# Kernel optimization log

Hardware: AMD Instinct MI355X
Metric: run time of the kernel (lower is better)

Reference implementation:

```python
import jax, jax.numpy as jnp
import numpy as np

L = 5        # n_layers
H = 8        # heads
DH = 32      # dim_head = n_hidden // heads
D = 256      # n_hidden
KR = 4       # key_ratio
QKD = KR * DH  # 128, q/k feature dim
IN = 3       # fun_dim + space_dim
OUT = 1      # out_dim
N = 32768    # number of mesh points
EPS = 1e-5

def _ln(x, g, b):
    m = jnp.mean(x, axis=-1, keepdims=True)
    v = jnp.var(x, axis=-1, keepdims=True)
    return (x - m) * jax.lax.rsqrt(v + EPS) * g + b

def _gelu(x):
    return jax.nn.gelu(x, approximate=False)  # torch nn.GELU default (erf)

def setup_inputs() -> dict:
    key = jax.random.key(0)
    ks = iter(jax.random.split(key, 64))
    def w(*s):
        return jax.random.normal(next(ks), s, jnp.float32) * 0.02
    return {
        "x": jax.random.normal(next(ks), (N, IN), jnp.float32),
        # preprocess MLP: Linear(IN,2D)+GELU, Linear(2D,D)
        "pre_w1": w(IN, 2 * D), "pre_b1": jnp.zeros((2 * D,), jnp.float32),
        "pre_w2": w(2 * D, D), "pre_b2": jnp.zeros((D,), jnp.float32),
        "placeholder": jax.random.uniform(next(ks), (D,), jnp.float32) / D,
        # per-block params stacked over L
        "ln1_g": jnp.ones((L, D), jnp.float32), "ln1_b": jnp.zeros((L, D), jnp.float32),
        "inp_w": w(L, D, D), "inp_b": jnp.zeros((L, D), jnp.float32),
        "temp_q": jnp.full((L, H), 0.5, jnp.float32), "temp_k": jnp.full((L, H), 0.5, jnp.float32),
        "wq": w(L, DH, QKD), "wk": w(L, DH, QKD), "wv": w(L, DH, DH),
        "out_w1": w(L, D, D), "out_b1": jnp.zeros((L, D), jnp.float32),
        "out_w2": w(L, D, D), "out_b2": jnp.zeros((L, D), jnp.float32),
        "ln2_g": jnp.ones((L, D), jnp.float32), "ln2_b": jnp.zeros((L, D), jnp.float32),
        "mlp_w1": w(L, D, D), "mlp_b1": jnp.zeros((L, D), jnp.float32),  # mlp_ratio=1 -> hidden=D
        "mlp_w2": w(L, D, D), "mlp_b2": jnp.zeros((L, D), jnp.float32),
        # last-layer head
        "ln3_g": jnp.ones((D,), jnp.float32), "ln3_b": jnp.zeros((D,), jnp.float32),
        "head_w": w(D, OUT), "head_b": jnp.zeros((OUT,), jnp.float32),
    }

def reference(x, pre_w1, pre_b1, pre_w2, pre_b2, placeholder,
              ln1_g, ln1_b, inp_w, inp_b, temp_q, temp_k, wq, wk, wv,
              out_w1, out_b1, out_w2, out_b2, ln2_g, ln2_b,
              mlp_w1, mlp_b1, mlp_w2, mlp_b2, ln3_g, ln3_b, head_w, head_b):
    # preprocess + placeholder bias
    fx = _gelu(x[None] @ pre_w1 + pre_b1) @ pre_w2 + pre_b2  # [1, N, D]
    fx = fx + placeholder
    for i in range(L):
        # --- LinearNO attention block ---
        h = _ln(fx, ln1_g[i], ln1_b[i])
        xm = h @ inp_w[i] + inp_b[i]                       # [1, N, D]
        xm = xm.reshape(1, N, H, DH).transpose(0, 2, 1, 3)  # [1, H, N, DH]
        q = jnp.einsum('bhnd,de->bhne', xm, wq[i])          # [1, H, N, QKD]
        k = jnp.einsum('bhnd,de->bhne', xm, wk[i])          # [1, H, N, QKD]
        v = jnp.einsum('bhnd,dc->bhnc', xm, wv[i])          # [1, H, N, DH]
        tq = jnp.clip(temp_q[i], 0.1, 2.0)[None, :, None, None]
        tk = jnp.clip(temp_k[i], 0.1, 2.0)[None, :, None, None]
        q = jax.nn.softmax(q / tq, axis=-1)  # over feature dim
        k = jax.nn.softmax(k / tk, axis=-2)  # over point dim
        kv = jnp.einsum('bhnd,bhnc->bhdc', k, v)    # [1, H, QKD, DH]
        qkv = jnp.einsum('bhnd,bhdc->bhnc', q, kv)  # [1, H, N, DH]
        qkv = qkv.transpose(0, 2, 1, 3).reshape(1, N, D)
        attn = _gelu(qkv @ out_w1[i] + out_b1[i]) @ out_w2[i] + out_b2[i]
        fx = attn + fx
        # --- MLP block (n_layers=0, res=False: pre + post only) ---
        h2 = _ln(fx, ln2_g[i], ln2_b[i])
        fx = _gelu(h2 @ mlp_w1[i] + mlp_b1[i]) @ mlp_w2[i] + mlp_b2[i] + fx
    # last block head: mlp2(ln_3(fx))
    out = _ln(fx, ln3_g, ln3_b) @ head_w + head_b  # [1, N, OUT]
    return out[0]  # module returns fx[0]
```

## Files before the change

kernel.cpp:

```cpp
#include <hip/hip_runtime.h>
#include <hip/hip_bf16.h>
#include <math.h>

constexpr int NP  = 32768;
constexpr int HH  = 8;

typedef short bf16x8 __attribute__((ext_vector_type(8)));
typedef float f32x4  __attribute__((ext_vector_type(4)));

__device__ __forceinline__ float gelu_f(float x) {
    return 0.5f * x * (1.0f + erff(x * 0.70710678118654752f));
}

__device__ __forceinline__ unsigned short f2bf(float x) {
    union { float f; unsigned u; } v; v.f = x;
    unsigned r = v.u + 0x7fffu + ((v.u >> 16) & 1u);
    return (unsigned short)(r >> 16);
}

__device__ __forceinline__ float bf2f(unsigned short h) {
    union { unsigned u; float f; } v; v.u = ((unsigned)h) << 16;
    return v.f;
}

// ... 117 lines not shown
            float4 s0 = *(const float4*)sp;
            float4 s1 = *(const float4*)(sp + 4);
            float mean = (s0.x + s0.z + s1.x + s1.z) * (1.f / 256.f);
            float ex2  = (s0.y + s0.w + s1.y + s1.w) * (1.f / 256.f);
            rmean[tid] = mean;
            rrstd[tid] = rsqrtf(fmaxf(ex2 - mean * mean, 0.f) + 1e-5f);
        }
        __syncthreads();
    }

    f32x4 acc[4][4];
    #pragma unroll
    for (int i = 0; i < 4; ++i)
        #pragma unroll
        for (int j = 0; j < 4; ++j)
            acc[i][j] = (f32x4){0.f, 0.f, 0.f, 0.f};

    const int lane = tid & 63, wid = tid >> 6;
    const int wr = wid >> 1, wc = wid & 1;
    const int lrow = lane & 15, quad = lane >> 4;
    const int srow = tid >> 3;
    const int sch  = tid & 7;

    for (int kc = 0; kc < K; kc += 64) {
        if constexpr (GENA) {
            #pragma unroll
            for (int it = 0; it < 4; ++it) {
                int row = srow + it * 32;
                float x0 = x3s[row * 4 + 0], x1 = x3s[row * 4 + 1], x2 = x3s[row * 4 + 2];
                unsigned short pk[8];
                #pragma unroll
                for (int j = 0; j < 8; ++j) {
                    int k = kc + sch * 8 + j;
                    float t = x0 * w1s[k] + x1 * w1s[512 + k] + x2 * w1s[1024 + k] + b1s[k];
                    pk[j] = f2bf(gelu_f(t));
                }
                *(uint4*)&As[row * 64 + ((sch ^ (row & 7)) << 3)] = *(uint4*)pk;
            }
        } else if constexpr (AF32) {
            #pragma unroll
            for (int it = 0; it < 4; ++it) {
                int row = srow + it * 32;
                const float* ap = Af + (size_t)(rBase + row) * K + kc + sch * 8;
                float4 a0 = *(const float4*)ap;
                float4 a1 = *(const float4*)(ap + 4);
                unsigned short pk[8];
                pk[0] = f2bf(a0.x); pk[1] = f2bf(a0.y); pk[2] = f2bf(a0.z); pk[3] = f2bf(a0.w);
                pk[4] = f2bf(a1.x); pk[5] = f2bf(a1.y); pk[6] = f2bf(a1.z); pk[7] = f2bf(a1.w);
                *(uint4*)&As[row * 64 + ((sch ^ (row & 7)) << 3)] = *(uint4*)pk;
            }
        } else {
            #pragma unroll
            for (int it = 0; it < 4; ++it) {
                int row = srow + it * 32;
                uint4 av = *(const uint4*)(Ah + (size_t)(rBase + row) * K + kc + sch * 8);
                *(uint4*)&As[row * 64 + ((sch ^ (row & 7)) << 3)] = av;
            }
        }
        #pragma unroll
        for (int it = 0; it < 4; ++it) {
            int n = srow + it * 32;
            uint4 wv_ = *(const uint4*)(Wt + (size_t)(cBase + n) * K + kc + sch * 8);
            *(uint4*)&Bs[n * 64 + ((sch ^ (n & 7)) << 3)] = wv_;
        }
        __syncthreads();
        #pragma unroll
        for (int ks = 0; ks < 2; ++ks) {
            bf16x8 af[4], bfr[4];
            #pragma unroll
            for (int t = 0; t < 4; ++t) {
                int row = wr * 64 + t * 16 + lrow;
                af[t] = *(bf16x8*)&As[row * 64 + (((ks * 4 + quad) ^ (row & 7)) << 3)];
                int n = wc * 64 + t * 16 + lrow;
                bfr[t] = *(bf16x8*)&Bs[n * 64 + (((ks * 4 + quad) ^ (n & 7)) << 3)];
            }
            #pragma unroll
            for (int ti = 0; ti < 4; ++ti)
                #pragma unroll
                for (int tj = 0; tj < 4; ++tj)
                    acc[ti][tj] = __builtin_amdgcn_mfma_f32_16x16x32_bf16(
                        af[ti], bfr[tj], acc[ti][tj], 0, 0, 0);
        }
        __syncthreads();
    }

    float c1b[4], c2r[4];
    #pragma unroll
    for (int tj = 0; tj < 4; ++tj) {
        int gcol = cBase + wc * 64 + tj * 16 + lrow;
        float b = bias[gcol];
        if (bias2) b += bias2[gcol];
        if constexpr (LNFOLD) {
            c1b[tj] = c1v[gcol] + b;
            c2r[tj] = c2vec[gcol];
        } else {
            c1b[tj] = b;
            c2r[tj] = 0.f;
        }
    }
    #pragma unroll
    for (int ti = 0; ti < 4; ++ti) {
        #pragma unroll
        for (int r = 0; r < 4; ++r) {
            int rib = wr * 64 + ti * 16 + quad * 4 + r;
            int grow = rBase + rib;
            float mean = 0.f, rstd = 1.f;
            if constexpr (LNFOLD) { mean = rmean[rib]; rstd = rrstd[rib]; }
            float vv[4];
            #pragma unroll
            for (int tj = 0; tj < 4; ++tj) {
                float t = acc[ti][tj][r];
                float v;
                if constexpr (LNFOLD) v = rstd * (t - mean * c2r[tj]) + c1b[tj];
                else                  v = t + c1b[tj];
                if constexpr (DOGELU) v = gelu_f(v);
                vv[tj] = v;
            }
            if constexpr (RESID) {
                #pragma unroll
                for (int tj = 0; tj < 4; ++tj) {
                    int gcol = cBase + wc * 64 + tj * 16 + lrow;
                    vv[tj] += outF[(size_t)grow * 256 + gcol];
                }
            }
            if constexpr (STATS) {
                float rs = vv[0] + vv[1] + vv[2] + vv[3];
                float rq = vv[0]*vv[0] + vv[1]*vv[1] + vv[2]*vv[2] + vv[3]*vv[3];
                #pragma unroll
                for (int m = 1; m < 16; m <<= 1) {
                    rs += __shfl_xor(rs, m);
                    rq += __shfl_xor(rq, m);
                }
                if (lrow == 0) {
                    stats_out[(size_t)grow * 8 + (blockIdx.y * 2 + wc) * 2 + 0] = rs;
                    stats_out[(size_t)grow * 8 + (blockIdx.y * 2 + wc) * 2 + 1] = rq;
                }
            }
            #pragma unroll
            for (int tj = 0; tj < 4; ++tj) {
                int gcol = cBase + wc * 64 + tj * 16 + lrow;
                if constexpr (PERM) {
                    size_t pidx = (size_t)(gcol >> 5) * NP * 32 + (size_t)grow * 32 + (gcol & 31);
                    if (outF) outF[pidx] = vv[tj];
                    if (outH) outH[pidx] = f2bf(vv[tj]);
                } else {
                    if (outF) outF[(size_t)grow * 256 + gcol] = vv[tj];
                    if (outH) outH[(size_t)grow * 256 + gcol] = f2bf(vv[tj]);
                }
            }
        }
    }
}

template<bool AF32, bool LNFOLD>
__global__ __launch_bounds__(256) void gemm_lgl(
    const unsigned short* __restrict__ Ah, const float* __restrict__ Af,
    const unsigned short* __restrict__ W1t, const unsigned short* __restrict__ W2t,
    const float* __restrict__ b1, const float* __restrict__ b2,
    float* __restrict__ fx,
    const float* __restrict__ stats_in, float* __restrict__ stats_out,
    const float* __restrict__ c1v, const float* __restrict__ c2vec)
{
    __shared__ __align__(16) unsigned short As[64 * 64];
    __shared__ __align__(16) unsigned short Bs[256 * 64];
    __shared__ __align__(16) unsigned short Ts[64 * 256];
    __shared__ float rmean[LNFOLD ? 64 : 1];
    __shared__ float rrstd[LNFOLD ? 64 : 1];

    const int tid = threadIdx.x;
    const int rBase = blockIdx.x * 64;
    const int lane = tid & 63, wid = tid >> 6;
    const int lrow = lane & 15, quad = lane >> 4;

    if constexpr (LNFOLD) {
        if (tid < 64) {
            const float* sp = stats_in + (size_t)(rBase + tid) * 8;
            float4 s0 = *(const float4*)sp;
            float4 s1 = *(const float4*)(sp + 4);
            float mean = (s0.x + s0.z + s1.x + s1.z) * (1.f / 256.f);
            float ex2  = (s0.y + s0.w + s1.y + s1.w) * (1.f / 256.f);
            rmean[tid] = mean;
            rrstd[tid] = rsqrtf(fmaxf(ex2 - mean * mean, 0.f) + 1e-5f);
        }
    }

    f32x4 acc[4][4];
    #pragma unroll
    for (int i = 0; i < 4; ++i)
        #pragma unroll
        for (int j = 0; j < 4; ++j)
            acc[i][j] = (f32x4){0.f, 0.f, 0.f, 0.f};

    for (int kc = 0; kc < 256; kc += 64) {
        #pragma unroll
        for (int it = 0; it < 2; ++it) {
            int idx = tid + it * 256;
            int row = idx >> 3, sch = idx & 7;
            if constexpr (AF32) {
                const float* ap = Af + (size_t)(rBase + row) * 256 + kc + sch * 8;
                float4 a0 = *(const float4*)ap;
                float4 a1 = *(const float4*)(ap + 4);
                unsigned short pk[8];
                pk[0] = f2bf(a0.x); pk[1] = f2bf(a0.y); pk[2] = f2bf(a0.z); pk[3] = f2bf(a0.w);
                pk[4] = f2bf(a1.x); pk[5] = f2bf(a1.y); pk[6] = f2bf(a1.z); pk[7] = f2bf(a1.w);
                *(uint4*)&As[row * 64 + ((sch ^ (row & 7)) << 3)] = *(uint4*)pk;
            } else {
                uint4 av = *(const uint4*)(Ah + (size_t)(rBase + row) * 256 + kc + sch * 8);
                *(uint4*)&As[row * 64 + ((sch ^ (row & 7)) << 3)] = av;
            }
        }
        #pragma unroll
        for (int it = 0; it < 8; ++it) {
            int idx = tid + it * 256;
            int n = idx >> 3, sch = idx & 7;
            uint4 wv_ = *(const uint4*)(W1t + (size_t)n * 256 + kc + sch * 8);
            *(uint4*)&Bs[n * 64 + ((sch ^ (n & 7)) << 3)] = wv_;
        }
        __syncthreads();
        #pragma unroll
        for (int ks = 0; ks < 2; ++ks) {
            bf16x8 af[4], bfr[4];
            #pragma unroll
            for (int t = 0; t < 4; ++t) {
                int row = t * 16 + lrow;
                af[t] = *(bf16x8*)&As[row * 64 + (((ks * 4 + quad) ^ (row & 7)) << 3)];
                int n = wid * 64 + t * 16 + lrow;
                bfr[t] = *(bf16x8*)&Bs[n * 64 + (((ks * 4 + quad) ^ (n & 7)) << 3)];
            }
            #pragma unroll
            for (int ti = 0; ti < 4; ++ti)
                #pragma unroll
                for (int tj = 0; tj < 4; ++tj)
                    acc[ti][tj] = __builtin_amdgcn_mfma_f32_16x16x32_bf16(
                        af[ti], bfr[tj], acc[ti][tj], 0, 0, 0);
        }
        __syncthreads();
    }

    {
        float c1b[4], c2r[4];
        #pragma unroll
        for (int tj = 0; tj < 4; ++tj) {
            int gcol = wid * 64 + tj * 16 + lrow;
            if constexpr (LNFOLD) {
                c1b[tj] = c1v[gcol] + b1[gcol];
                c2r[tj] = c2vec[gcol];
            } else {
                c1b[tj] = b1[gcol];
                c2r[tj] = 0.f;
            }
        }
        #pragma unroll
        for (int ti = 0; ti < 4; ++ti) {
            #pragma unroll
            for (int r = 0; r < 4; ++r) {
                int row = ti * 16 + quad * 4 + r;
                float mean = 0.f, rstd = 1.f;
                if constexpr (LNFOLD) { mean = rmean[row]; rstd = rrstd[row]; }
                #pragma unroll
                for (int tj = 0; tj < 4; ++tj) {
                    float t = acc[ti][tj][r];
                    float v;
                    if constexpr (LNFOLD) v = rstd * (t - mean * c2r[tj]) + c1b[tj];
                    else                  v = t + c1b[tj];
                    v = gelu_f(v);
                    int col = wid * 64 + tj * 16 + lrow;
                    int ch = col >> 3;
                    Ts[row * 256 + ((ch ^ (row & 7)) << 3) + (col & 7)] = f2bf(v);
                }
            }
        }
    }
    __syncthreads();

    f32x4 acc2[4][4];
    #pragma unroll
    for (int i = 0; i < 4; ++i)
        #pragma unroll
        for (int j = 0; j < 4; ++j)
            acc2[i][j] = (f32x4){0.f, 0.f, 0.f, 0.f};

    for (int kc = 0; kc < 256; kc += 64) {
        #pragma unroll
        for (int it = 0; it < 8; ++it) {
            int idx = tid + it * 256;
            int n = idx >> 3, sch = idx & 7;
            uint4 wv_ = *(const uint4*)(W2t + (size_t)n * 256 + kc + sch * 8);
            *(uint4*)&Bs[n * 64 + ((sch ^ (n & 7)) << 3)] = wv_;
        }
        __syncthreads();
        #pragma unroll
        for (int ks = 0; ks < 2; ++ks) {
            bf16x8 af[4], bfr[4];
            #pragma unroll
            for (int t = 0; t < 4; ++t) {
                int row = t * 16 + lrow;
                int ch = (kc >> 3) + ks * 4 + quad;
                af[t] = *(bf16x8*)&Ts[row * 256 + ((ch ^ (row & 7)) << 3)];
                int n = wid * 64 + t * 16 + lrow;
                bfr[t] = *(bf16x8*)&Bs[n * 64 + (((ks * 4 + quad) ^ (n & 7)) << 3)];
            }
            #pragma unroll
            for (int ti = 0; ti < 4; ++ti)
                #pragma unroll
                for (int tj = 0; tj < 4; ++tj)
                    acc2[ti][tj] = __builtin_amdgcn_mfma_f32_16x16x32_bf16(
                        af[ti], bfr[tj], acc2[ti][tj], 0, 0, 0);
        }
        __syncthreads();
    }

    float bb[4];
    #pragma unroll
    for (int tj = 0; tj < 4; ++tj) bb[tj] = b2[wid * 64 + tj * 16 + lrow];
    #pragma unroll
    for (int ti = 0; ti < 4; ++ti) {
        #pragma unroll
        for (int r = 0; r < 4; ++r) {
            int grow = rBase + ti * 16 + quad * 4 + r;
            float vv[4];
            #pragma unroll
            for (int tj = 0; tj < 4; ++tj) {
                int gcol = wid * 64 + tj * 16 + lrow;
                vv[tj] = acc2[ti][tj][r] + bb[tj] + fx[(size_t)grow * 256 + gcol];
            }
            float rs = vv[0] + vv[1] + vv[2] + vv[3];
            float rq = vv[0]*vv[0] + vv[1]*vv[1] + vv[2]*vv[2] + vv[3]*vv[3];
            #pragma unroll
            for (int m = 1; m < 16; m <<= 1) {
                rs += __shfl_xor(rs, m);
                rq += __shfl_xor(rq, m);
            }
            if (lrow == 0) {
                stats_out[(size_t)grow * 8 + wid * 2 + 0] = rs;
                stats_out[(size_t)grow * 8 + wid * 2 + 1] = rq;
            }
            #pragma unroll
            for (int tj = 0; tj < 4; ++tj) {
                int gcol = wid * 64 + tj * 16 + lrow;
                fx[(size_t)grow * 256 + gcol] = vv[tj];
            }
        }
    }
}

__global__ __launch_bounds__(256) void kv6_kernel(
    const unsigned short* __restrict__ xm2h, const unsigned short* __restrict__ wkT,
    const unsigned short* __restrict__ wvT, const float* __restrict__ tk_arr,
    float* __restrict__ partials, int layer)
{
    __shared__ __align__(16) unsigned short xs[64 * 32];
    __shared__ __align__(16) unsigned short wks[128 * 32];
    __shared__ __align__(16) unsigned short wvs[32 * 32];
    __shared__ __align__(16) unsigned short els[128 * 72];
    __shared__ __align__(16) unsigned short vls[32 * 72];
    __shared__ float sums[4 * 128];

    const int tid = threadIdx.x;
    const int h = blockIdx.y;
    const int rowBase = blockIdx.x * 512;
    const int w = tid >> 6, lane = tid & 63;
    const int lrow = lane & 15, quad = lane >> 4;

    float tk = fminf(fmaxf(tk_arr[layer * 8 + h], 0.1f), 2.0f);
    float invtk = 1.0f / tk;

    #pragma unroll
    for (int it = 0; it < 2; ++it) {
        int cid = tid + it * 256;
        int d = cid >> 2, kc = cid & 3;
        uint4 v = *(const uint4*)(wkT + d * 32 + kc * 8);
        *(uint4*)&wks[d * 32 + ((kc ^ (d & 3)) << 3)] = v;
    }
    if (tid < 128) {
        int c = tid >> 2, kc = tid & 3;
        uint4 v = *(const uint4*)(wvT + c * 32 + kc * 8);
        *(uint4*)&wvs[c * 32 + ((kc ^ (c & 3)) << 3)] = v;
    }

    f32x4 acc2[2][2];
    #pragma unroll
    for (int di = 0; di < 2; ++di)
        #pragma unroll
        for (int ci = 0; ci < 2; ++ci)
            acc2[di][ci] = (f32x4){0.f, 0.f, 0.f, 0.f};
    float seacc[8];
    #pragma unroll
    for (int dt = 0; dt < 8; ++dt) seacc[dt] = 0.f;

    const unsigned short* src = xm2h + (size_t)h * NP * 32 + (size_t)rowBase * 32;

    for (int sub = 0; sub < 8; ++sub) {
        __syncthreads();
        {
            int row = tid >> 2, kc = tid & 3;
            uint4 v = *(const uint4*)(src + (size_t)(sub * 64 + row) * 32 + kc * 8);
            *(uint4*)&xs[row * 32 + ((kc ^ (row & 3)) << 3)] = v;
        }
        __syncthreads();
        int arow = w * 16 + lrow;
        bf16x8 ax = *(bf16x8*)&xs[arow * 32 + ((quad ^ (arow & 3)) << 3)];
        #pragma unroll
        for (int ct = 0; ct < 2; ++ct) {
            int c = ct * 16 + lrow;
            bf16x8 bw = *(bf16x8*)&wvs[c * 32 + ((quad ^ (c & 3)) << 3)];
            f32x4 cc = (f32x4){0.f, 0.f, 0.f, 0.f};
            cc = __builtin_amdgcn_mfma_f32_16x16x32_bf16(ax, bw, cc, 0, 0, 0);
            unsigned short pk[4];
            pk[0] = f2bf(cc[0]); pk[1] = f2bf(cc[1]);
            pk[2] = f2bf(cc[2]); pk[3] = f2bf(cc[3]);
            *(uint2*)&vls[(ct * 16 + lrow) * 72 + w * 16 + quad * 4] = *(uint2*)pk;
        }
        #pragma unroll
        for (int dt = 0; dt < 8; ++dt) {
            int d = dt * 16 + lrow;
            bf16x8 bw = *(bf16x8*)&wks[d * 32 + ((quad ^ (d & 3)) << 3)];
            f32x4 cc = (f32x4){0.f, 0.f, 0.f, 0.f};
            cc = __builtin_amdgcn_mfma_f32_16x16x32_bf16(ax, bw, cc, 0, 0, 0);
            unsigned short pk[4];
            float se = 0.f;
            #pragma unroll
            for (int r = 0; r < 4; ++r) {
                float l = fminf(fmaxf(cc[r] * invtk, -30.f), 30.f);
                unsigned short eb = f2bf(__expf(l));
                pk[r] = eb;
                se += bf2f(eb);
            }
            seacc[dt] += se;
            *(uint2*)&els[d * 72 + w * 16 + quad * 4] = *(uint2*)pk;
        }
        __syncthreads();
        #pragma unroll
        for (int di = 0; di < 2; ++di) {
            int dm = (2 * w + di) * 16 + lrow;
            #pragma unroll
            for (int ks = 0; ks < 2; ++ks) {
                bf16x8 ae = *(bf16x8*)&els[dm * 72 + ks * 32 + quad * 8];
                #pragma unroll
                for (int ci = 0; ci < 2; ++ci) {
                    int cn = ci * 16 + lrow;
                    bf16x8 bv = *(bf16x8*)&vls[cn * 72 + ks * 32 + quad * 8];
                    acc2[di][ci] = __builtin_amdgcn_mfma_f32_16x16x32_bf16(
                        ae, bv, acc2[di][ci], 0, 0, 0);
                }
            }
        }
    }

    float* outp = partials + ((size_t)h * 64 + blockIdx.x) * 4224;
    #pragma unroll
    for (int di = 0; di < 2; ++di)
        #pragma unroll
        for (int ci = 0; ci < 2; ++ci)
            #pragma unroll
            for (int r = 0; r < 4; ++r) {
                int d = (2 * w + di) * 16 + quad * 4 + r;
                int c = ci * 16 + lrow;
                outp[d * 32 + c] = acc2[di][ci][r];
            }
    #pragma unroll
    for (int dt = 0; dt < 8; ++dt) {
        float s = seacc[dt];
        s += __shfl_xor(s, 16);
        s += __shfl_xor(s, 32);
        if (quad == 0) sums[w * 128 + dt * 16 + lrow] = s;
    }
    __syncthreads();
    if (tid < 128)
        outp[4096 + tid] = sums[tid] + sums[128 + tid] + sums[256 + tid] + sums[384 + tid];
}

__global__ __launch_bounds__(256) void kv_reduce_kernel(
    const float* __restrict__ partials, unsigned short* __restrict__ kvT,
    float* __restrict__ sumexp)
{
    int gid = blockIdx.x * 256 + threadIdx.x;
    if (gid >= 8 * 4224) return;
    int h = gid / 4224, idx = gid % 4224;
    const float* base = partials + (size_t)h * 64 * 4224 + idx;
    float s = 0.f;
    #pragma unroll 8
    for (int c = 0; c < 64; ++c) s += base[(size_t)c * 4224];
    if (idx < 4096) {
        int d = idx >> 5, c = idx & 31;
        kvT[(size_t)h * 4096 + c * 128 + d] = f2bf(s);
    } else {
        sumexp[h * 128 + (idx - 4096)] = s;
    }
}

__global__ __launch_bounds__(256) void qkv6_kernel(
    const unsigned short* __restrict__ xm2h, const unsigned short* __restrict__ wqT,
    const float* __restrict__ tq_arr, const unsigned short* __restrict__ kvT,
    const float* __restrict__ sumexp, unsigned short* __restrict__ outH, int layer)
{
    __shared__ __align__(16) unsigned short xs[64 * 32];
    __shared__ __align__(16) unsigned short wqs[128 * 32];
    __shared__ __align__(16) unsigned short kvb[32 * 136];
    __shared__ __align__(16) unsigned short els[64 * 136];
    __shared__ float ises[128];

    const int tid = threadIdx.x;
    const int h = blockIdx.y;
    const int rowBase = blockIdx.x * 64;
    const int w = tid >> 6, lane = tid & 63;
    const int lrow = lane & 15, quad = lane >> 4;

    float tq = fminf(fmaxf(tq_arr[layer * 8 + h], 0.1f), 2.0f);
    float invtq = 1.0f / tq;

    if (tid < 128) ises[tid] = 1.0f / sumexp[h * 128 + tid];
    #pragma unroll
    for (int it = 0; it < 2; ++it) {
        int cid = tid + it * 256;
        int d = cid >> 2, kc = cid & 3;
        uint4 v = *(const uint4*)(wqT + d * 32 + kc * 8);
        *(uint4*)&wqs[d * 32 + ((kc ^ (d & 3)) << 3)] = v;
    }
    #pragma unroll
    for (int it = 0; it < 2; ++it) {
        int cid = tid + it * 256;
        int c = cid >> 4, k8 = cid & 15;
        uint4 v = *(const uint4*)(kvT + (size_t)h * 4096 + c * 128 + k8 * 8);
        *(uint4*)&kvb[c * 136 + k8 * 8] = v;
    }
    {
        int row = tid >> 2, kc = tid & 3;
        uint4 v = *(const uint4*)(xm2h + (size_t)h * NP * 32 +
                                  (size_t)(rowBase + row) * 32 + kc * 8);
        *(uint4*)&xs[row * 32 + ((kc ^ (row & 3)) << 3)] = v;
    }
    __syncthreads();

    int arow = w * 16 + lrow;
    bf16x8 ax = *(bf16x8*)&xs[arow * 32 + ((quad ^ (arow & 3)) << 3)];
    f32x4 lg[8];
    #pragma unroll
    for (int dt = 0; dt < 8; ++dt) {
        int d = dt * 16 + lrow;
        bf16x8 bw = *(bf16x8*)&wqs[d * 32 + ((quad ^ (d & 3)) << 3)];
        f32x4 cc = (f32x4){0.f, 0.f, 0.f, 0.f};
        lg[dt] = __builtin_amdgcn_mfma_f32_16x16x32_bf16(ax, bw, cc, 0, 0, 0);
    }
    float isv[8];
    #pragma unroll
    for (int dt = 0; dt < 8; ++dt) isv[dt] = ises[dt * 16 + lrow];

    #pragma unroll
    for (int r = 0; r < 4; ++r) {
        float m = lg[0][r];
        #pragma unroll
        for (int dt = 1; dt < 8; ++dt) m = fmaxf(m, lg[dt][r]);
        m = fmaxf(m, __shfl_xor(m, 1));
        m = fmaxf(m, __shfl_xor(m, 2));
        m = fmaxf(m, __shfl_xor(m, 4));
        m = fmaxf(m, __shfl_xor(m, 8));
        float e[8], s = 0.f;
        #pragma unroll
        for (int dt = 0; dt < 8; ++dt) {
            e[dt] = __expf((lg[dt][r] - m) * invtq);
            s += e[dt];
        }
        s += __shfl_xor(s, 1);
        s += __shfl_xor(s, 2);
        s += __shfl_xor(s, 4);
        s += __shfl_xor(s, 8);
        float inv = 1.0f / s;
        int erow = w * 16 + quad * 4 + r;
        #pragma unroll
        for (int dt = 0; dt < 8; ++dt)
            els[erow * 136 + dt * 16 + lrow] = f2bf(e[dt] * inv * isv[dt]);
    }

    #pragma unroll
    for (int ct = 0; ct < 2; ++ct) {
        f32x4 oc = (f32x4){0.f, 0.f, 0.f, 0.f};
        #pragma unroll
        for (int ks = 0; ks < 4; ++ks) {
            bf16x8 ae = *(bf16x8*)&els[(w * 16 + lrow) * 136 + ks * 32 + quad * 8];
            bf16x8 bv = *(bf16x8*)&kvb[(ct * 16 + lrow) * 136 + ks * 32 + quad * 8];
            oc = __builtin_amdgcn_mfma_f32_16x16x32_bf16(ae, bv, oc, 0, 0, 0);
        }
        #pragma unroll
        for (int r = 0; r < 4; ++r)
            outH[(size_t)(rowBase + w * 16 + quad * 4 + r) * 256 +
                 h * 32 + ct * 16 + lrow] = f2bf(oc[r]);
    }
}

__global__ __launch_bounds__(256) void head_kernel(
    const float* __restrict__ fx, const float* __restrict__ g, const float* __restrict__ b,
    const float* __restrict__ hw, const float* __restrict__ hb, float* __restrict__ out)
{
    int lane = threadIdx.x & 63;
    int row = blockIdx.x * 4 + (threadIdx.x >> 6);
    float4 v = *(const float4*)(fx + (size_t)row * 256 + lane * 4);
    float s1 = v.x + v.y + v.z + v.w;
    float s2 = v.x * v.x + v.y * v.y + v.z * v.z + v.w * v.w;
    #pragma unroll
    for (int m = 1; m < 64; m <<= 1) { s1 += __shfl_xor(s1, m); s2 += __shfl_xor(s2, m); }
    float mean = s1 * 0.00390625f;
    float rstd = rsqrtf(fmaxf(s2 * 0.00390625f - mean * mean, 0.f) + 1e-5f);
    float4 gg = *(const float4*)(g + lane * 4);
    float4 bb = *(const float4*)(b + lane * 4);
    float4 w4 = *(const float4*)(hw + lane * 4);
    float d = ((v.x - mean) * rstd * gg.x + bb.x) * w4.x
            + ((v.y - mean) * rstd * gg.y + bb.y) * w4.y
            + ((v.z - mean) * rstd * gg.z + bb.z) * w4.z
            + ((v.w - mean) * rstd * gg.w + bb.w) * w4.w;
    #pragma unroll
    for (int m = 1; m < 64; m <<= 1) d += __shfl_xor(d, m);
    if (lane == 0) out[row] = d + hb[0];
}

extern "C" void kernel_launch(void* const* d_in, const int* in_sizes, int n_in,
                              void* d_out, int out_size, void* d_ws, size_t ws_size,
                              hipStream_t stream)
{
    const float* x      = (const float*)d_in[0];
    const float* pre_w1 = (const float*)d_in[1];
    const float* pre_b1 = (const float*)d_in[2];
    const float* pre_w2 = (const float*)d_in[3];
    const float* pre_b2 = (const float*)d_in[4];
    const float* ph     = (const float*)d_in[5];
    const float* ln1_g  = (const float*)d_in[6];
    const float* ln1_b  = (const float*)d_in[7];
    const float* inp_w  = (const float*)d_in[8];
    const float* inp_b  = (const float*)d_in[9];
    const float* temp_q = (const float*)d_in[10];
    const float* temp_k = (const float*)d_in[11];
    const float* wq     = (const float*)d_in[12];
    const float* wk     = (const float*)d_in[13];
    const float* wv     = (const float*)d_in[14];
    const float* out_w1 = (const float*)d_in[15];
    const float* out_b1 = (const float*)d_in[16];
    const float* out_w2 = (const float*)d_in[17];
    const float* out_b2 = (const float*)d_in[18];
    const float* ln2_g  = (const float*)d_in[19];
    const float* ln2_b  = (const float*)d_in[20];
    const float* mlp_w1 = (const float*)d_in[21];
    const float* mlp_b1 = (const float*)d_in[22];
    const float* mlp_w2 = (const float*)d_in[23];
    const float* mlp_b2 = (const float*)d_in[24];
    const float* ln3_g  = (const float*)d_in[25];
    const float* ln3_b  = (const float*)d_in[26];
    const float* head_w = (const float*)d_in[27];
    const float* head_b = (const float*)d_in[28];
    float* out = (float*)d_out;

    float* fx = (float*)d_ws;
    unsigned short* fxh = (unsigned short*)(fx + (size_t)NP * 256);
    unsigned short* ChH = fxh + (size_t)NP * 256;
    unsigned short* xm2h = ChH;
    float* scr = (float*)(ChH + (size_t)NP * 256);
    float* st = scr + (size_t)NP * 256;
    unsigned short* kvT = (unsigned short*)(st + (size_t)NP * 8);
    float* se = (float*)(kvT + 8 * 4096);
    float* c1i = se + 8 * 128;
    float* c2i = c1i + 1280;
    float* c1m = c2i + 1280;
    float* c2m = c1m + 1280;
    unsigned short* wtPre = (unsigned short*)(c2m + 1280);
    unsigned short* wtL   = wtPre + 256 * 512;
    unsigned short* wkT   = wtL + 25 * 65536;
    unsigned short* wvT   = wkT + 5 * 4096;
    unsigned short* wqT   = wvT + 5 * 1024;

    unsigned short* wtIn = wtL;
    unsigned short* wtO1 = wtL +  5 * 65536;
    unsigned short* wtO2 = wtL + 10 * 65536;
    unsigned short* wtM1 = wtL + 15 * 65536;
    unsigned short* wtM2 = wtL + 20 * 65536;

    unsigned short* qh = (unsigned short*)scr;

    dim3 bt(256);

    transpose_bf16_k<<<dim3(16, 8, 1), bt, 0, stream>>>(pre_w2, wtPre, 512);
    transpose_scale_bf16_k<<<dim3(8, 8, 5), bt, 0, stream>>>(inp_w,  ln1_g, wtIn, 256);
    transpose_bf16_k<<<dim3(8, 8, 5), bt, 0, stream>>>(out_w1, wtO1, 256);
    transpose_bf16_k<<<dim3(8, 8, 5), bt, 0, stream>>>(out_w2, wtO2, 256);
    transpose_scale_bf16_k<<<dim3(8, 8, 5), bt, 0, stream>>>(mlp_w1, ln2_g, wtM1, 256);
    transpose_bf16_k<<<dim3(8, 8, 5), bt, 0, stream>>>(mlp_w2, wtM2, 256);
    colsum_k<<<dim3(1, 1, 5), bt, 0, stream>>>(inp_w,  ln1_g, ln1_b, c2i, c1i);
    colsum_k<<<dim3(1, 1, 5), bt, 0, stream>>>(mlp_w1, ln2_g, ln2_b, c2m, c1m);
    prep_wkvT<<<dim3(5), bt, 0, stream>>>(wk, wv, wq, wkT, wvT, wqT);

    dim3 gg(256, 2);

    gemm_bf<true, false, false, false, false, true, false><<<gg, bt, 0, stream>>>(
        nullptr, nullptr, wtPre, pre_b2, ph, fx, nullptr, nullptr, st,
        nullptr, nullptr, x, pre_w1, pre_b1, 512);

    for (int i = 0; i < 5; ++i) {
        gemm_bf<false, true, true, false, false, false, true><<<gg, bt, 0, stream>>>(
            nullptr, fx, wtIn + (size_t)i * 65536, inp_b + i * 256, nullptr, nullptr, xm2h,
            st, nullptr, c1i + i * 256, c2i + i * 256, nullptr, nullptr, nullptr, 256);
        kv6_kernel<<<dim3(64, 8), bt, 0, stream>>>(
            xm2h, wkT + (size_t)i * 4096, wvT + (size_t)i * 1024, temp_k, scr, i);
        kv_reduce_kernel<<<dim3(132), bt, 0, stream>>>(scr, kvT, se);
        qkv6_kernel<<<dim3(512, 8), bt, 0, stream>>>(
            xm2h, wqT + (size_t)i * 4096, temp_q, kvT, se, qh, i);
        gemm_lgl<false, false><<<dim3(512), bt, 0, stream>>>(
            qh, nullptr, wtO1 + (size_t)i * 65536, wtO2 + (size_t)i * 65536,
            out_b1 + i * 256, out_b2 + i * 256, fx, nullptr, st, nullptr, nullptr);
        gemm_lgl<true, true><<<dim3(512), bt, 0, stream>>>(
            nullptr, fx, wtM1 + (size_t)i * 65536, wtM2 + (size_t)i * 65536,
            mlp_b1 + i * 256, mlp_b2 + i * 256, fx, st, st,
            c1m + i * 256, c2m + i * 256);
    }
    head_kernel<<<dim3(NP / 4), bt, 0, stream>>>(fx, ln3_g, ln3_b, head_w, head_b, out);
}
```

Baseline: 830.5 us.

## Fuse q-softmax attention, out-MLP, LN-MLP and next-layer input projection into one kernel

Replaces the qkv6 kernel and the two gemm_lgl launches with a single per-64-row mega kernel. It computes the q softmax times kv for all 8 heads into shared memory, then runs the out-projection MLP, the residual with in-kernel LayerNorm statistics, the MLP block, and the next layer's LN-folded input projection. The xm buffers are double-buffered across layers. This removes the global round trips for the qkv output, the fx reread, the stats and several launches, at the cost of higher shared memory and register pressure, which may lower occupancy.

```diff
diff --git a/kernel.cpp b/kernel.cpp
--- a/kernel.cpp
+++ b/kernel.cpp
@@ -293,103 +293,169 @@
     }
 }
 
-template<bool AF32, bool LNFOLD>
-__global__ __launch_bounds__(256) void gemm_lgl(
-    const unsigned short* __restrict__ Ah, const float* __restrict__ Af,
-    const unsigned short* __restrict__ W1t, const unsigned short* __restrict__ W2t,
-    const float* __restrict__ b1, const float* __restrict__ b2,
+template<bool NEXTW>
+__global__ __launch_bounds__(256, 2) void mega_kernel(
+    const unsigned short* __restrict__ xm,
+    const unsigned short* __restrict__ wqT,
+    const float* __restrict__ tq_arr,
+    const unsigned short* __restrict__ kvT,
+    const float* __restrict__ sumexp,
+    const unsigned short* __restrict__ O1t, const float* __restrict__ ob1,
+    const unsigned short* __restrict__ O2t, const float* __restrict__ ob2,
+    const unsigned short* __restrict__ M1t, const float* __restrict__ mb1,
+    const unsigned short* __restrict__ M2t, const float* __restrict__ mb2,
+    const float* __restrict__ c1m, const float* __restrict__ c2m,
     float* __restrict__ fx,
-    const float* __restrict__ stats_in, float* __restrict__ stats_out,
-    const float* __restrict__ c1v, const float* __restrict__ c2vec)
+    const unsigned short* __restrict__ W3t, const float* __restrict__ b3,
+    const float* __restrict__ c1n, const float* __restrict__ c2n,
+    unsigned short* __restrict__ outNext, int layer)
 {
-    __shared__ __align__(16) unsigned short As[64 * 64];
-    __shared__ __align__(16) unsigned short Bs[256 * 64];
+    __shared__ __align__(16) unsigned char upool[38912];
     __shared__ __align__(16) unsigned short Ts[64 * 256];
-    __shared__ float rmean[LNFOLD ? 64 : 1];
-    __shared__ float rrstd[LNFOLD ? 64 : 1];
+    __shared__ float rmean[64];
+    __shared__ float rrstd[64];
+    __shared__ float ssum[256];
+    __shared__ float ssq[256];
+
+    unsigned short* xs  = (unsigned short*)(upool);
+    unsigned short* wqs = (unsigned short*)(upool + 4096);
+    unsigned short* kvb = (unsigned short*)(upool + 12288);
+    unsigned short* els = (unsigned short*)(upool + 20992);
+    float*          ises = (float*)(upool + 38400);
+    unsigned short* Bs  = (unsigned short*)(upool);
 
     const int tid = threadIdx.x;
     const int rBase = blockIdx.x * 64;
     const int lane = tid & 63, wid = tid >> 6;
     const int lrow = lane & 15, quad = lane >> 4;
 
-    if constexpr (LNFOLD) {
-        if (tid < 64) {
-            const float* sp = stats_in + (size_t)(rBase + tid) * 8;
-            float4 s0 = *(const float4*)sp;
-            float4 s1 = *(const float4*)(sp + 4);
-            float mean = (s0.x + s0.z + s1.x + s1.z) * (1.f / 256.f);
-            float ex2  = (s0.y + s0.w + s1.y + s1.w) * (1.f / 256.f);
-            rmean[tid] = mean;
-            rrstd[tid] = rsqrtf(fmaxf(ex2 - mean * mean, 0.f) + 1e-5f);
-        }
-    }
-
-    f32x4 acc[4][4];
-    #pragma unroll
-    for (int i = 0; i < 4; ++i)
-        #pragma unroll
-        for (int j = 0; j < 4; ++j)
-            acc[i][j] = (f32x4){0.f, 0.f, 0.f, 0.f};
-
-    for (int kc = 0; kc < 256; kc += 64) {
+    #pragma unroll
+    for (int it = 0; it < 2; ++it) {
+        int cid = tid + it * 256;
+        int d = cid >> 2, kc = cid & 3;
+        uint4 v = *(const uint4*)(wqT + d * 32 + kc * 8);
+        *(uint4*)&wqs[d * 32 + ((kc ^ (d & 3)) << 3)] = v;
+    }
+    for (int h = 0; h < 8; ++h) {
+        if (h) __syncthreads();
+        float tq = fminf(fmaxf(tq_arr[layer * 8 + h], 0.1f), 2.0f);
+        float invtq = 1.0f / tq;
+        if (tid < 128) ises[tid] = 1.0f / sumexp[h * 128 + tid];
         #pragma unroll
         for (int it = 0; it < 2; ++it) {
-            int idx = tid + it * 256;
-            int row = idx >> 3, sch = idx & 7;
-            if constexpr (AF32) {
-                const float* ap = Af + (size_t)(rBase + row) * 256 + kc + sch * 8;
-                float4 a0 = *(const float4*)ap;
-                float4 a1 = *(const float4*)(ap + 4);
-                unsigned short pk[8];
-                pk[0] = f2bf(a0.x); pk[1] = f2bf(a0.y); pk[2] = f2bf(a0.z); pk[3] = f2bf(a0.w);
-                pk[4] = f2bf(a1.x); pk[5] = f2bf(a1.y); pk[6] = f2bf(a1.z); pk[7] = f2bf(a1.w);
-                *(uint4*)&As[row * 64 + ((sch ^ (row & 7)) << 3)] = *(uint4*)pk;
-            } else {
-                uint4 av = *(const uint4*)(Ah + (size_t)(rBase + row) * 256 + kc + sch * 8);
-                *(uint4*)&As[row * 64 + ((sch ^ (row & 7)) << 3)] = av;
-            }
-        }
-        #pragma unroll
-        for (int it = 0; it < 8; ++it) {
-            int idx = tid + it * 256;
-            int n = idx >> 3, sch = idx & 7;
-            uint4 wv_ = *(const uint4*)(W1t + (size_t)n * 256 + kc + sch * 8);
-            *(uint4*)&Bs[n * 64 + ((sch ^ (n & 7)) << 3)] = wv_;
+            int cid = tid + it * 256;
+            int c = cid >> 4, k8 = cid & 15;
+            uint4 v = *(const uint4*)(kvT + (size_t)h * 4096 + c * 128 + k8 * 8);
+            *(uint4*)&kvb[c * 136 + k8 * 8] = v;
+        }
+        {
+            int row = tid >> 2, kc = tid & 3;
+            uint4 v = *(const uint4*)(xm + (size_t)h * NP * 32 +
+                                      (size_t)(rBase + row) * 32 + kc * 8);
+            *(uint4*)&xs[row * 32 + ((kc ^ (row & 3)) << 3)] = v;
         }
         __syncthreads();
-        #pragma unroll
-        for (int ks = 0; ks < 2; ++ks) {
-            bf16x8 af[4], bfr[4];
-            #pragma unroll
-            for (int t = 0; t < 4; ++t) {
-                int row = t * 16 + lrow;
-                af[t] = *(bf16x8*)&As[row * 64 + (((ks * 4 + quad) ^ (row & 7)) << 3)];
-                int n = wid * 64 + t * 16 + lrow;
-                bfr[t] = *(bf16x8*)&Bs[n * 64 + (((ks * 4 + quad) ^ (n & 7)) << 3)];
-            }
-            #pragma unroll
-            for (int ti = 0; ti < 4; ++ti)
-                #pragma unroll
-                for (int tj = 0; tj < 4; ++tj)
-                    acc[ti][tj] = __builtin_amdgcn_mfma_f32_16x16x32_bf16(
-                        af[ti], bfr[tj], acc[ti][tj], 0, 0, 0);
-        }
-        __syncthreads();
-    }
-
-    {
+
+        int arow = wid * 16 + lrow;
+        bf16x8 ax = *(bf16x8*)&xs[arow * 32 + ((quad ^ (arow & 3)) << 3)];
+        f32x4 lg[8];
+        #pragma unroll
+        for (int dt = 0; dt < 8; ++dt) {
+            int d = dt * 16 + lrow;
+            bf16x8 bw = *(bf16x8*)&wqs[d * 32 + ((quad ^ (d & 3)) << 3)];
+            f32x4 cc = (f32x4){0.f, 0.f, 0.f, 0.f};
+            lg[dt] = __builtin_amdgcn_mfma_f32_16x16x32_bf16(ax, bw, cc, 0, 0, 0);
+        }
+        float isv[8];
+        #pragma unroll
+        for (int dt = 0; dt < 8; ++dt) isv[dt] = ises[dt * 16 + lrow];
+
+        #pragma unroll
+        for (int r = 0; r < 4; ++r) {
+            float m = lg[0][r];
+            #pragma unroll
+            for (int dt = 1; dt < 8; ++dt) m = fmaxf(m, lg[dt][r]);
+            m = fmaxf(m, __shfl_xor(m, 1));
+            m = fmaxf(m, __shfl_xor(m, 2));
+            m = fmaxf(m, __shfl_xor(m, 4));
+            m = fmaxf(m, __shfl_xor(m, 8));
+            float e[8], s = 0.f;
+            #pragma unroll
+            for (int dt = 0; dt < 8; ++dt) {
+                e[dt] = __expf((lg[dt][r] - m) * invtq);
+                s += e[dt];
+            }
+            s += __shfl_xor(s, 1);
+            s += __shfl_xor(s, 2);
+            s += __shfl_xor(s, 4);
+            s += __shfl_xor(s, 8);
+            float inv = 1.0f / s;
+            int erow = wid * 16 + quad * 4 + r;
+            #pragma unroll
+            for (int dt = 0; dt < 8; ++dt)
+                els[erow * 136 + dt * 16 + lrow] = f2bf(e[dt] * inv * isv[dt]);
+        }
+
+        #pragma unroll
+        for (int ct = 0; ct < 2; ++ct) {
+            f32x4 oc = (f32x4){0.f, 0.f, 0.f, 0.f};
+            #pragma unroll
+            for (int ks = 0; ks < 4; ++ks) {
+                bf16x8 ae = *(bf16x8*)&els[(wid * 16 + lrow) * 136 + ks * 32 + quad * 8];
+                bf16x8 bv = *(bf16x8*)&kvb[(ct * 16 + lrow) * 136 + ks * 32 + quad * 8];
+                oc = __builtin_amdgcn_mfma_f32_16x16x32_bf16(ae, bv, oc, 0, 0, 0);
+            }
+            #pragma unroll
+            for (int r = 0; r < 4; ++r) {
+                int row = wid * 16 + quad * 4 + r;
+                int col = h * 32 + ct * 16 + lrow;
+                int ch = col >> 3;
+                Ts[row * 256 + ((ch ^ (row & 7)) << 3) + (col & 7)] = f2bf(oc[r]);
+            }
+        }
+    }
+    __syncthreads();
+
+    auto gemm_phase = [&](const unsigned short* __restrict__ Wt, f32x4 (&acc)[4][4]) {
+        for (int kc = 0; kc < 256; kc += 64) {
+            #pragma unroll
+            for (int it = 0; it < 8; ++it) {
+                int idx = tid + it * 256;
+                int n = idx >> 3, sch = idx & 7;
+                uint4 wv_ = *(const uint4*)(Wt + (size_t)n * 256 + kc + sch * 8);
+                *(uint4*)&Bs[n * 64 + ((sch ^ (n & 7)) << 3)] = wv_;
+            }
+            __syncthreads();
+            #pragma unroll
+            for (int ks = 0; ks < 2; ++ks) {
+                bf16x8 af[4], bfr[4];
+                #pragma unroll
+                for (int t = 0; t < 4; ++t) {
+                    int row = t * 16 + lrow;
+                    int ch = (kc >> 3) + ks * 4 + quad;
+                    af[t] = *(bf16x8*)&Ts[row * 256 + ((ch ^ (row & 7)) << 3)];
+                    int n = wid * 64 + t * 16 + lrow;
+                    bfr[t] = *(bf16x8*)&Bs[n * 64 + (((ks * 4 + quad) ^ (n & 7)) << 3)];
+                }
+                #pragma unroll
+                for (int ti = 0; ti < 4; ++ti)
+                    #pragma unroll
+                    for (int tj = 0; tj < 4; ++tj)
+                        acc[ti][tj] = __builtin_amdgcn_mfma_f32_16x16x32_bf16(
+                            af[ti], bfr[tj], acc[ti][tj], 0, 0, 0);
+            }
+            __syncthreads();
+        }
+    };
+    auto epi_gelu = [&](f32x4 (&acc)[4][4], const float* __restrict__ bias,
+                        const float* __restrict__ c1vv, const float* __restrict__ c2vv,
+                        bool lnfold) {
         float c1b[4], c2r[4];
         #pragma unroll
         for (int tj = 0; tj < 4; ++tj) {
             int gcol = wid * 64 + tj * 16 + lrow;
-            if constexpr (LNFOLD) {
-                c1b[tj] = c1v[gcol] + b1[gcol];
-                c2r[tj] = c2vec[gcol];
-            } else {
-                c1b[tj] = b1[gcol];
-                c2r[tj] = 0.f;
-            }
+            if (lnfold) { c1b[tj] = c1vv[gcol] + bias[gcol]; c2r[tj] = c2vv[gcol]; }
+            else        { c1b[tj] = bias[gcol];              c2r[tj] = 0.f; }
         }
         #pragma unroll
         for (int ti = 0; ti < 4; ++ti) {
@@ -397,13 +463,13 @@
             for (int r = 0; r < 4; ++r) {
                 int row = ti * 16 + quad * 4 + r;
                 float mean = 0.f, rstd = 1.f;
-                if constexpr (LNFOLD) { mean = rmean[row]; rstd = rrstd[row]; }
+                if (lnfold) { mean = rmean[row]; rstd = rrstd[row]; }
                 #pragma unroll
                 for (int tj = 0; tj < 4; ++tj) {
                     float t = acc[ti][tj][r];
                     float v;
-                    if constexpr (LNFOLD) v = rstd * (t - mean * c2r[tj]) + c1b[tj];
-                    else                  v = t + c1b[tj];
+                    if (lnfold) v = rstd * (t - mean * c2r[tj]) + c1b[tj];
+                    else        v = t + c1b[tj];
                     v = gelu_f(v);
                     int col = wid * 64 + tj * 16 + lrow;
                     int ch = col >> 3;
@@ -411,75 +477,153 @@
                 }
             }
         }
+    };
+
+    f32x4 acc[4][4];
+    #pragma unroll
+    for (int i = 0; i < 4; ++i)
+        #pragma unroll
+        for (int j = 0; j < 4; ++j) acc[i][j] = (f32x4){0.f, 0.f, 0.f, 0.f};
+    gemm_phase(O1t, acc);
+    epi_gelu(acc, ob1, nullptr, nullptr, false);
+
+    #pragma unroll
+    for (int i = 0; i < 4; ++i)
+        #pragma unroll
+        for (int j = 0; j < 4; ++j) acc[i][j] = (f32x4){0.f, 0.f, 0.f, 0.f};
+    gemm_phase(O2t, acc);
+
+    float fxm[4][4][4];
+    {
+        float bb[4];
+        #pragma unroll
+        for (int tj = 0; tj < 4; ++tj) bb[tj] = ob2[wid * 64 + tj * 16 + lrow];
+        #pragma unroll
+        for (int ti = 0; ti < 4; ++ti) {
+            #pragma unroll
+            for (int r = 0; r < 4; ++r) {
+                int row = ti * 16 + quad * 4 + r;
+                int grow = rBase + row;
+                #pragma unroll
+                for (int tj = 0; tj < 4; ++tj) {
+                    int gcol = wid * 64 + tj * 16 + lrow;
+                    fxm[ti][r][tj] = acc[ti][tj][r] + bb[tj] + fx[(size_t)grow * 256 + gcol];
+                }
+                float rs = fxm[ti][r][0] + fxm[ti][r][1] + fxm[ti][r][2] + fxm[ti][r][3];
+                float rq = fxm[ti][r][0]*fxm[ti][r][0] + fxm[ti][r][1]*fxm[ti][r][1]
+                         + fxm[ti][r][2]*fxm[ti][r][2] + fxm[ti][r][3]*fxm[ti][r][3];
+                #pragma unroll
+                for (int m = 1; m < 16; m <<= 1) {
+                    rs += __shfl_xor(rs, m);
+                    rq += __shfl_xor(rq, m);
+                }
+                if (lrow == 0) { ssum[row * 4 + wid] = rs; ssq[row * 4 + wid] = rq; }
+                #pragma unroll
+                for (int tj = 0; tj < 4; ++tj) {
+                    int gcol = wid * 64 + tj * 16 + lrow;
+                    int ch = gcol >> 3;
+                    Ts[row * 256 + ((ch ^ (row & 7)) << 3) + (gcol & 7)] = f2bf(fxm[ti][r][tj]);
+                }
+            }
+        }
     }
     __syncthreads();
-
-    f32x4 acc2[4][4];
+    if (tid < 64) {
+        float mean = (ssum[tid*4+0] + ssum[tid*4+1] + ssum[tid*4+2] + ssum[tid*4+3]) * (1.f/256.f);
+        float ex2  = (ssq [tid*4+0] + ssq [tid*4+1] + ssq [tid*4+2] + ssq [tid*4+3]) * (1.f/256.f);
+        rmean[tid] = mean;
+        rrstd[tid] = rsqrtf(fmaxf(ex2 - mean * mean, 0.f) + 1e-5f);
+    }
+    __syncthreads();
+
     #pragma unroll
     for (int i = 0; i < 4; ++i)
         #pragma unroll
-        for (int j = 0; j < 4; ++j)
-            acc2[i][j] = (f32x4){0.f, 0.f, 0.f, 0.f};
-
-    for (int kc = 0; kc < 256; kc += 64) {
-        #pragma unroll
-        for (int it = 0; it < 8; ++it) {
-            int idx = tid + it * 256;
-            int n = idx >> 3, sch = idx & 7;
-            uint4 wv_ = *(const uint4*)(W2t + (size_t)n * 256 + kc + sch * 8);
-            *(uint4*)&Bs[n * 64 + ((sch ^ (n & 7)) << 3)] = wv_;
-        }
+        for (int j = 0; j < 4; ++j) acc[i][j] = (f32x4){0.f, 0.f, 0.f, 0.f};
+    gemm_phase(M1t, acc);
+    epi_gelu(acc, mb1, c1m, c2m, true);
+
+    #pragma unroll
+    for (int i = 0; i < 4; ++i)
+        #pragma unroll
+        for (int j = 0; j < 4; ++j) acc[i][j] = (f32x4){0.f, 0.f, 0.f, 0.f};
+    gemm_phase(M2t, acc);
+    {
+        float bb[4];
+        #pragma unroll
+        for (int tj = 0; tj < 4; ++tj) bb[tj] = mb2[wid * 64 + tj * 16 + lrow];
+        #pragma unroll
+        for (int ti = 0; ti < 4; ++ti) {
+            #pragma unroll
+            for (int r = 0; r < 4; ++r) {
+                int row = ti * 16 + quad * 4 + r;
+                int grow = rBase + row;
+                float vv[4];
+                #pragma unroll
+                for (int tj = 0; tj < 4; ++tj)
+                    vv[tj] = acc[ti][tj][r] + bb[tj] + fxm[ti][r][tj];
+                if constexpr (NEXTW) {
+                    float rs = vv[0] + vv[1] + vv[2] + vv[3];
+                    float rq = vv[0]*vv[0] + vv[1]*vv[1] + vv[2]*vv[2] + vv[3]*vv[3];
+                    #pragma unroll
+                    for (int m = 1; m < 16; m <<= 1) {
+                        rs += __shfl_xor(rs, m);
+                        rq += __shfl_xor(rq, m);
+                    }
+                    if (lrow == 0) { ssum[row * 4 + wid] = rs; ssq[row * 4 + wid] = rq; }
+                }
+                #pragma unroll
+                for (int tj = 0; tj < 4; ++tj) {
+                    int gcol = wid * 64 + tj * 16 + lrow;
+                    fx[(size_t)grow * 256 + gcol] = vv[tj];
+                    if constexpr (NEXTW) {
+                        int ch = gcol >> 3;
+                        Ts[row * 256 + ((ch ^ (row & 7)) << 3) + (gcol & 7)] = f2bf(vv[tj]);
+                    }
+                }
+            }
+        }
+    }
+
+    if constexpr (NEXTW) {
         __syncthreads();
-        #pragma unroll
-        for (int ks = 0; ks < 2; ++ks) {
-            bf16x8 af[4], bfr[4];
-            #pragma unroll
-            for (int t = 0; t < 4; ++t) {
-                int row = t * 16 + lrow;
-                int ch = (kc >> 3) + ks * 4 + quad;
-                af[t] = *(bf16x8*)&Ts[row * 256 + ((ch ^ (row & 7)) << 3)];
-                int n = wid * 64 + t * 16 + lrow;
-                bfr[t] = *(bf16x8*)&Bs[n * 64 + (((ks * 4 + quad) ^ (n & 7)) << 3)];
-            }
-            #pragma unroll
-            for (int ti = 0; ti < 4; ++ti)
-                #pragma unroll
-                for (int tj = 0; tj < 4; ++tj)
-                    acc2[ti][tj] = __builtin_amdgcn_mfma_f32_16x16x32_bf16(
-                        af[ti], bfr[tj], acc2[ti][tj], 0, 0, 0);
+        if (tid < 64) {
+            float mean = (ssum[tid*4+0] + ssum[tid*4+1] + ssum[tid*4+2] + ssum[tid*4+3]) * (1.f/256.f);
+            float ex2  = (ssq [tid*4+0] + ssq [tid*4+1] + ssq [tid*4+2] + ssq [tid*4+3]) * (1.f/256.f);
+            rmean[tid] = mean;
+            rrstd[tid] = rsqrtf(fmaxf(ex2 - mean * mean, 0.f) + 1e-5f);
         }
         __syncthreads();
-    }
-
-    float bb[4];
-    #pragma unroll
-    for (int tj = 0; tj < 4; ++tj) bb[tj] = b2[wid * 64 + tj * 16 + lrow];
-    #pragma unroll
-    for (int ti = 0; ti < 4; ++ti) {
-        #pragma unroll
-        for (int r = 0; r < 4; ++r) {
-            int grow = rBase + ti * 16 + quad * 4 + r;
-            float vv[4];
-            #pragma unroll
-            for (int tj = 0; tj < 4; ++tj) {
-                int gcol = wid * 64 + tj * 16 + lrow;
-                vv[tj] = acc2[ti][tj][r] + bb[tj] + fx[(size_t)grow * 256 + gcol];
-            }
-            float rs = vv[0] + vv[1] + vv[2] + vv[3];
-            float rq = vv[0]*vv[0] + vv[1]*vv[1] + vv[2]*vv[2] + vv[3]*vv[3];
-            #pragma unroll
-            for (int m = 1; m < 16; m <<= 1) {
-                rs += __shfl_xor(rs, m);
-                rq += __shfl_xor(rq, m);
-            }
-            if (lrow == 0) {
-                stats_out[(size_t)grow * 8 + wid * 2 + 0] = rs;
-                stats_out[(size_t)grow * 8 + wid * 2 + 1] = rq;
-            }
-            #pragma unroll
-            for (int tj = 0; tj < 4; ++tj) {
-                int gcol = wid * 64 + tj * 16 + lrow;
-                fx[(size_t)grow * 256 + gcol] = vv[tj];
+
+        f32x4 acc5[4][4];
+        #pragma unroll
+        for (int i = 0; i < 4; ++i)
+            #pragma unroll
+            for (int j = 0; j < 4; ++j) acc5[i][j] = (f32x4){0.f, 0.f, 0.f, 0.f};
+        gemm_phase(W3t, acc5);
+
+        float c1b3[4], c2r3[4];
+        #pragma unroll
+        for (int tj = 0; tj < 4; ++tj) {
+            int gcol = wid * 64 + tj * 16 + lrow;
+            c1b3[tj] = c1n[gcol] + b3[gcol];
+            c2r3[tj] = c2n[gcol];
+        }
+        #pragma unroll
+        for (int ti = 0; ti < 4; ++ti) {
+            #pragma unroll
+            for (int r = 0; r < 4; ++r) {
+                int row = ti * 16 + quad * 4 + r;
+                int grow = rBase + row;
+                float mean = rmean[row], rstd = rrstd[row];
+                #pragma unroll
+                for (int tj = 0; tj < 4; ++tj) {
+                    int gcol = wid * 64 + tj * 16 + lrow;
+                    float t = acc5[ti][tj][r];
+                    float v = rstd * (t - mean * c2r3[tj]) + c1b3[tj];
+                    size_t pidx = (size_t)(gcol >> 5) * NP * 32 + (size_t)grow * 32 + (gcol & 31);
+                    outNext[pidx] = f2bf(v);
+                }
             }
         }
     }
@@ -627,105 +771,6 @@
         kvT[(size_t)h * 4096 + c * 128 + d] = f2bf(s);
     } else {
         sumexp[h * 128 + (idx - 4096)] = s;
-    }
-}
-
-__global__ __launch_bounds__(256) void qkv6_kernel(
-    const unsigned short* __restrict__ xm2h, const unsigned short* __restrict__ wqT,
-    const float* __restrict__ tq_arr, const unsigned short* __restrict__ kvT,
-    const float* __restrict__ sumexp, unsigned short* __restrict__ outH, int layer)
-{
-    __shared__ __align__(16) unsigned short xs[64 * 32];
-    __shared__ __align__(16) unsigned short wqs[128 * 32];
-    __shared__ __align__(16) unsigned short kvb[32 * 136];
-    __shared__ __align__(16) unsigned short els[64 * 136];
-    __shared__ float ises[128];
-
-    const int tid = threadIdx.x;
-    const int h = blockIdx.y;
-    const int rowBase = blockIdx.x * 64;
-    const int w = tid >> 6, lane = tid & 63;
-    const int lrow = lane & 15, quad = lane >> 4;
-
-    float tq = fminf(fmaxf(tq_arr[layer * 8 + h], 0.1f), 2.0f);
-    float invtq = 1.0f / tq;
-
-    if (tid < 128) ises[tid] = 1.0f / sumexp[h * 128 + tid];
-    #pragma unroll
-    for (int it = 0; it < 2; ++it) {
-        int cid = tid + it * 256;
-        int d = cid >> 2, kc = cid & 3;
-        uint4 v = *(const uint4*)(wqT + d * 32 + kc * 8);
-        *(uint4*)&wqs[d * 32 + ((kc ^ (d & 3)) << 3)] = v;
-    }
-    #pragma unroll
-    for (int it = 0; it < 2; ++it) {
-        int cid = tid + it * 256;
-        int c = cid >> 4, k8 = cid & 15;
-        uint4 v = *(const uint4*)(kvT + (size_t)h * 4096 + c * 128 + k8 * 8);
-        *(uint4*)&kvb[c * 136 + k8 * 8] = v;
-    }
-    {
-        int row = tid >> 2, kc = tid & 3;
-        uint4 v = *(const uint4*)(xm2h + (size_t)h * NP * 32 +
-                                  (size_t)(rowBase + row) * 32 + kc * 8);
-        *(uint4*)&xs[row * 32 + ((kc ^ (row & 3)) << 3)] = v;
-    }
-    __syncthreads();
-
-    int arow = w * 16 + lrow;
-    bf16x8 ax = *(bf16x8*)&xs[arow * 32 + ((quad ^ (arow & 3)) << 3)];
-    f32x4 lg[8];
-    #pragma unroll
-    for (int dt = 0; dt < 8; ++dt) {
-        int d = dt * 16 + lrow;
-        bf16x8 bw = *(bf16x8*)&wqs[d * 32 + ((quad ^ (d & 3)) << 3)];
-        f32x4 cc = (f32x4){0.f, 0.f, 0.f, 0.f};
-        lg[dt] = __builtin_amdgcn_mfma_f32_16x16x32_bf16(ax, bw, cc, 0, 0, 0);
-    }
-    float isv[8];
-    #pragma unroll
-    for (int dt = 0; dt < 8; ++dt) isv[dt] = ises[dt * 16 + lrow];
-
-    #pragma unroll
-    for (int r = 0; r < 4; ++r) {
-        float m = lg[0][r];
-        #pragma unroll
-        for (int dt = 1; dt < 8; ++dt) m = fmaxf(m, lg[dt][r]);
-        m = fmaxf(m, __shfl_xor(m, 1));
-        m = fmaxf(m, __shfl_xor(m, 2));
-        m = fmaxf(m, __shfl_xor(m, 4));
-        m = fmaxf(m, __shfl_xor(m, 8));
-        float e[8], s = 0.f;
-        #pragma unroll
-        for (int dt = 0; dt < 8; ++dt) {
-            e[dt] = __expf((lg[dt][r] - m) * invtq);
-            s += e[dt];
-        }
-        s += __shfl_xor(s, 1);
-        s += __shfl_xor(s, 2);
-        s += __shfl_xor(s, 4);
-        s += __shfl_xor(s, 8);
-        float inv = 1.0f / s;
-        int erow = w * 16 + quad * 4 + r;
-        #pragma unroll
-        for (int dt = 0; dt < 8; ++dt)
-            els[erow * 136 + dt * 16 + lrow] = f2bf(e[dt] * inv * isv[dt]);
-    }
-
-    #pragma unroll
-    for (int ct = 0; ct < 2; ++ct) {
-        f32x4 oc = (f32x4){0.f, 0.f, 0.f, 0.f};
-        #pragma unroll
-        for (int ks = 0; ks < 4; ++ks) {
-            bf16x8 ae = *(bf16x8*)&els[(w * 16 + lrow) * 136 + ks * 32 + quad * 8];
-            bf16x8 bv = *(bf16x8*)&kvb[(ct * 16 + lrow) * 136 + ks * 32 + quad * 8];
-            oc = __builtin_amdgcn_mfma_f32_16x16x32_bf16(ae, bv, oc, 0, 0, 0);
-        }
-        #pragma unroll
-        for (int r = 0; r < 4; ++r)
-            outH[(size_t)(rowBase + w * 16 + quad * 4 + r) * 256 +
-                 h * 32 + ct * 16 + lrow] = f2bf(oc[r]);
     }
 }
 
@@ -790,10 +835,9 @@
     float* out = (float*)d_out;
 
     float* fx = (float*)d_ws;
-    unsigned short* fxh = (unsigned short*)(fx + (size_t)NP * 256);
-    unsigned short* ChH = fxh + (size_t)NP * 256;
-    unsigned short* xm2h = ChH;
-    float* scr = (float*)(ChH + (size_t)NP * 256);
+    unsigned short* xmB = (unsigned short*)(fx + (size_t)NP * 256);
+    unsigned short* xmA = xmB + (size_t)NP * 256;
+    float* scr = (float*)(xmA + (size_t)NP * 256);
     float* st = scr + (size_t)NP * 256;
     unsigned short* kvT = (unsigned short*)(st + (size_t)NP * 8);
     float* se = (float*)(kvT + 8 * 4096);
@@ -813,8 +857,6 @@
     unsigned short* wtM1 = wtL + 15 * 65536;
     unsigned short* wtM2 = wtL + 20 * 65536;
 
-    unsigned short* qh = (unsigned short*)scr;
-
     dim3 bt(256);
 
     transpose_bf16_k<<<dim3(16, 8, 1), bt, 0, stream>>>(pre_w2, wtPre, 512);
@@ -833,22 +875,36 @@
         nullptr, nullptr, wtPre, pre_b2, ph, fx, nullptr, nullptr, st,
         nullptr, nullptr, x, pre_w1, pre_b1, 512);
 
+    gemm_bf<false, true, true, false, false, false, true><<<gg, bt, 0, stream>>>(
+        nullptr, fx, wtIn, inp_b, nullptr, nullptr, xmA,
+        st, nullptr, c1i, c2i, nullptr, nullptr, nullptr, 256);
+
     for (int i = 0; i < 5; ++i) {
-        gemm_bf<false, true, true, false, false, false, true><<<gg, bt, 0, stream>>>(
-            nullptr, fx, wtIn + (size_t)i * 65536, inp_b + i * 256, nullptr, nullptr, xm2h,
-            st, nullptr, c1i + i * 256, c2i + i * 256, nullptr, nullptr, nullptr, 256);
+        unsigned short* xmCur  = (i & 1) ? xmB : xmA;
+        unsigned short* xmNext = (i & 1) ? xmA : xmB;
         kv6_kernel<<<dim3(64, 8), bt, 0, stream>>>(
-            xm2h, wkT + (size_t)i * 4096, wvT + (size_t)i * 1024, temp_k, scr, i);
+            xmCur, wkT + (size_t)i * 4096, wvT + (size_t)i * 1024, temp_k, scr, i);
         kv_reduce_kernel<<<dim3(132), bt, 0, stream>>>(scr, kvT, se);
-        qkv6_kernel<<<dim3(512, 8), bt, 0, stream>>>(
-            xm2h, wqT + (size_t)i * 4096, temp_q, kvT, se, qh, i);
-        gemm_lgl<false, false><<<dim3(512), bt, 0, stream>>>(
-            qh, nullptr, wtO1 + (size_t)i * 65536, wtO2 + (size_t)i * 65536,
-            out_b1 + i * 256, out_b2 + i * 256, fx, nullptr, st, nullptr, nullptr);
-        gemm_lgl<true, true><<<dim3(512), bt, 0, stream>>>(
-            nullptr, fx, wtM1 + (size_t)i * 65536, wtM2 + (size_t)i * 65536,
-            mlp_b1 + i * 256, mlp_b2 + i * 256, fx, st, st,
-            c1m + i * 256, c2m + i * 256);
+        if (i < 4) {
+            mega_kernel<true><<<dim3(512), bt, 0, stream>>>(
+                xmCur, wqT + (size_t)i * 4096, temp_q, kvT, se,
+                wtO1 + (size_t)i * 65536, out_b1 + i * 256,
+                wtO2 + (size_t)i * 65536, out_b2 + i * 256,
+                wtM1 + (size_t)i * 65536, mlp_b1 + i * 256,
+                wtM2 + (size_t)i * 65536, mlp_b2 + i * 256,
+                c1m + i * 256, c2m + i * 256, fx,
+                wtIn + (size_t)(i + 1) * 65536, inp_b + (i + 1) * 256,
+                c1i + (i + 1) * 256, c2i + (i + 1) * 256, xmNext, i);
+        } else {
+            mega_kernel<false><<<dim3(512), bt, 0, stream>>>(
+                xmCur, wqT + (size_t)i * 4096, temp_q, kvT, se,
+                wtO1 + (size_t)i * 65536, out_b1 + i * 256,
+                wtO2 + (size_t)i * 65536, out_b2 + i * 256,
+                wtM1 + (size_t)i * 65536, mlp_b1 + i * 256,
+                wtM2 + (size_t)i * 65536, mlp_b2 + i * 256,
+                c1m + i * 256, c2m + i * 256, fx,
+                nullptr, nullptr, nullptr, nullptr, nullptr, i);
+        }
     }
     head_kernel<<<dim3(NP / 4), bt, 0, stream>>>(fx, ln3_g, ln3_b, head_w, head_b, out);
 }
```

Result: slower. 1.077 ms (+29.6%).
